# Kernel optimization log

Hardware: AMD Instinct MI355X
Metric: run time of the kernel (lower is better)

## Reference

```python
import math
import jax, jax.numpy as jnp
import numpy as np

DIM = 1024
N_HEADS = 16
N_KV_HEADS = 4
HEAD_DIM = 64
WINDOW = 512
EPS = 1e-6
B, S = 2, 2048

def _alibi_slopes(n_heads):
    def pow2(n):
        r = 2.0 ** (-8.0 / n)
        return np.array([r ** (i + 1) for i in range(n)], dtype=np.float32)
    if math.log2(n_heads).is_integer():
        return pow2(n_heads)
    m = 2 ** math.floor(math.log2(n_heads))
    return np.concatenate([pow2(m), pow2(2 * m)[::2][: n_heads - m]])

def _rmsnorm(x, w, eps=EPS):
    var = jnp.mean(x * x, axis=-1, keepdims=True)
    return x * jax.lax.rsqrt(var + eps) * w

def setup_inputs() -> dict:
    key = jax.random.key(0)
    ks = jax.random.split(key, 8)
    x = jax.random.normal(ks[0], (B, S, DIM), dtype=jnp.float32)
    wq = 0.02 * jax.random.normal(ks[1], (N_HEADS * HEAD_DIM, DIM), dtype=jnp.float32)
    wk = 0.02 * jax.random.normal(ks[2], (N_KV_HEADS * HEAD_DIM, DIM), dtype=jnp.float32)
    wv = 0.02 * jax.random.normal(ks[3], (N_KV_HEADS * HEAD_DIM, DIM), dtype=jnp.float32)
    wo = 0.02 * jax.random.normal(ks[4], (DIM, N_HEADS * HEAD_DIM), dtype=jnp.float32)
    q_norm_w = jnp.ones((N_HEADS * HEAD_DIM,), dtype=jnp.float32)
    k_norm_w = jnp.ones((N_KV_HEADS * HEAD_DIM,), dtype=jnp.float32)
    return {"x": x, "wq": wq, "wk": wk, "wv": wv, "wo": wo,
            "q_norm_w": q_norm_w, "k_norm_w": k_norm_w}

def reference(x, wq, wk, wv, wo, q_norm_w, k_norm_w):
    bsz, seqlen, _ = x.shape
    repeats = N_HEADS // N_KV_HEADS
    xq = _rmsnorm(x @ wq.T, q_norm_w)
    xk = _rmsnorm(x @ wk.T, k_norm_w)
    xv = x @ wv.T
    # [b, h, s, d]
    q = xq.reshape(bsz, seqlen, N_HEADS, HEAD_DIM).transpose(0, 2, 1, 3)
    k = xk.reshape(bsz, seqlen, N_KV_HEADS, HEAD_DIM).transpose(0, 2, 1, 3)
    v = xv.reshape(bsz, seqlen, N_KV_HEADS, HEAD_DIM).transpose(0, 2, 1, 3)
    k = jnp.repeat(k, repeats, axis=1)
    v = jnp.repeat(v, repeats, axis=1)
    pos = jnp.arange(seqlen)
    rel = pos[None, :] - pos[:, None]  # [s_q, s_k], key - query
    slopes = jnp.asarray(_alibi_slopes(N_HEADS))
    bias = slopes[:, None, None] * rel[None].astype(x.dtype)  # [h, s, s]
    masked = (rel > 0) | (rel < -WINDOW)  # causal + sliding window
    bias = jnp.where(masked[None], -jnp.inf, bias)
    scale = 1.0 / math.sqrt(HEAD_DIM)
    scores = jnp.einsum('bhqd,bhkd->bhqk', q, k) * scale + bias[None]
    probs = jax.nn.softmax(scores, axis=-1)
    y = jnp.einsum('bhqk,bhkd->bhqd', probs, v)
    y = y.transpose(0, 2, 1, 3).reshape(bsz, seqlen, N_HEADS * HEAD_DIM)
    return y @ wo.T
```

## Files before the change

### kernel.cpp

```cpp
#include <hip/hip_runtime.h>

typedef unsigned short u16;
typedef unsigned int u32;

typedef __bf16 bf16x8 __attribute__((ext_vector_type(8)));
typedef float f32x4 __attribute__((ext_vector_type(4)));

__device__ __forceinline__ u16 f2bf(float f) {
  u32 u = __builtin_bit_cast(u32, f);
  u32 r = (u + 0x7fffu + ((u >> 16) & 1u)) >> 16;
  return (u16)r;
}
__device__ __forceinline__ float bf2f(u16 v) {
  u32 u = (u32)v << 16;
  return __builtin_bit_cast(float, u);
}

__global__ __launch_bounds__(256)
void cvt_all_kernel(const float* __restrict__ x, const float* __restrict__ wq,
                    const float* __restrict__ wk, const float* __restrict__ wv,
                    const float* __restrict__ wo, u16* __restrict__ x_bf,
                    u16* __restrict__ wcat_bf, u16* __restrict__ wo_bf) {
  int t = blockIdx.x * 256 + threadIdx.x;
  const float* src;
  u16* dst;
  if (t < 1048576) {
    src = x; dst = x_bf;
  } else if (t < 1310720) {
    src = wq; dst = wcat_bf; t -= 1048576;
  } else if (t < 1376256) {
    src = wk; dst = wcat_bf + 1048576; t -= 1310720;
  } else if (t < 1441792) {
    src = wv; dst = wcat_bf + 1310720; t -= 1376256;
  } else {
    src = wo; dst = wo_bf; t -= 1441792;
  }
  const int i = t * 4;
  float4 v = *(const float4*)(src + i);
  uint2 p;
  p.x = (u32)f2bf(v.x) | ((u32)f2bf(v.y) << 16);
  p.y = (u32)f2bf(v.z) | ((u32)f2bf(v.w) << 16);
  *(uint2*)(dst + i) = p;
}

template <typename OutT>
__global__ __launch_bounds__(256)
void gemm_bt_kernel(const u16* __restrict__ A, const u16* __restrict__ B,
                    OutT* __restrict__ C, int M, int N, int K) {
  __shared__ u16 As[2][64 * 64];
  __shared__ u16 Bs[2][128 * 64];
  const int tid = threadIdx.x;
  const int lane = tid & 63;
  const int wave = tid >> 6;
  const int wm = (wave >> 1) * 32;
  const int wn = (wave & 1) * 64;
  const int l15 = lane & 15;
  const int quad = lane >> 4;
  const int sw = l15 & 7;
  const size_t bm = (size_t)blockIdx.y * 64;
  const size_t bn = (size_t)blockIdx.x * 128;

  f32x4 acc[2][4];
#pragma unroll
  for (int i = 0; i < 2; ++i)
#pragma unroll
    for (int j = 0; j < 4; ++j) acc[i][j] = f32x4{0.f, 0.f, 0.f, 0.f};

  const int ra0 = tid >> 3, ba0 = tid & 7;
  const int ra1 = (tid + 256) >> 3, ba1 = tid & 7;
  const u16* Ap0 = A + (bm + ra0) * (size_t)K + ba0 * 8;
  const u16* Ap1 = A + (bm + ra1) * (size_t)K + ba1 * 8;
  const u16* Bp0 = B + (bn + ra0) * (size_t)K + ba0 * 8;
  const u16* Bp1 = B + (bn + ra1) * (size_t)K + ba1 * 8;
  const u16* Bp2 = B + (bn + ra0 + 64) * (size_t)K + ba0 * 8;
  const u16* Bp3 = B + (bn + ra1 + 64) * (size_t)K + ba1 * 8;
  const int wa0 = ra0 * 64 + ((ba0 ^ (ra0 & 7)) * 8);
  const int wa1 = ra1 * 64 + ((ba1 ^ (ra1 & 7)) * 8);
  const int wb2 = (ra0 + 64) * 64 + ((ba0 ^ (ra0 & 7)) * 8);
  const int wb3 = (ra1 + 64) * 64 + ((ba1 ^ (ra1 & 7)) * 8);

  {
    uint4 a0 = *(const uint4*)Ap0, a1 = *(const uint4*)Ap1;
    uint4 b0 = *(const uint4*)Bp0, b1 = *(const uint4*)Bp1;
    uint4 b2 = *(const uint4*)Bp2, b3 = *(const uint4*)Bp3;
    *(uint4*)(&As[0][wa0]) = a0;
    *(uint4*)(&As[0][wa1]) = a1;
    *(uint4*)(&Bs[0][wa0]) = b0;
    *(uint4*)(&Bs[0][wa1]) = b1;
    *(uint4*)(&Bs[0][wb2]) = b2;
    *(uint4*)(&Bs[0][wb3]) = b3;
  }
  __syncthreads();

  int cur = 0;
  for (int k0 = 0; k0 < K; k0 += 64) {
    const int kn = (k0 + 64 < K) ? k0 + 64 : 0;
    uint4 a0 = *(const uint4*)(Ap0 + kn);
    uint4 a1 = *(const uint4*)(Ap1 + kn);
    uint4 b0 = *(const uint4*)(Bp0 + kn);
    uint4 b1 = *(const uint4*)(Bp1 + kn);
    uint4 b2 = *(const uint4*)(Bp2 + kn);
    uint4 b3 = *(const uint4*)(Bp3 + kn);

    const u16* Asc = As[cur];
    const u16* Bsc = Bs[cur];
#pragma unroll
    for (int h = 0; h < 2; ++h) {
      const int cb = quad + 4 * h;
      bf16x8 af[2], bfr[4];
#pragma unroll
      for (int i = 0; i < 2; ++i)
        af[i] = *(const bf16x8*)(&Asc[(wm + i * 16 + l15) * 64 + ((cb ^ sw) * 8)]);
#pragma unroll
      for (int j = 0; j < 4; ++j)
        bfr[j] = *(const bf16x8*)(&Bsc[(wn + j * 16 + l15) * 64 + ((cb ^ sw) * 8)]);
#pragma unroll
      for (int i = 0; i < 2; ++i)
#pragma unroll
        for (int j = 0; j < 4; ++j)
          acc[i][j] = __builtin_amdgcn_mfma_f32_16x16x32_bf16(af[i], bfr[j], acc[i][j], 0, 0, 0);
    }

    u16* Asn = As[cur ^ 1];
    u16* Bsn = Bs[cur ^ 1];
    *(uint4*)(&Asn[wa0]) = a0;
    *(uint4*)(&Asn[wa1]) = a1;
    *(uint4*)(&Bsn[wa0]) = b0;
    *(uint4*)(&Bsn[wa1]) = b1;
    *(uint4*)(&Bsn[wb2]) = b2;
    *(uint4*)(&Bsn[wb3]) = b3;
    __syncthreads();
    cur ^= 1;
  }

  const int rq = quad * 4;
#pragma unroll
  for (int i = 0; i < 2; ++i) {
#pragma unroll
    for (int r = 0; r < 4; ++r) {
      OutT* crow = C + (bm + wm + i * 16 + rq + r) * (size_t)N + bn + wn + l15;
#pragma unroll
      for (int j = 0; j < 4; ++j) {
        if constexpr (sizeof(OutT) == 2)
          crow[j * 16] = f2bf(acc[i][j][r]);
        else
          crow[j * 16] = acc[i][j][r];
      }
    }
  }
}

__global__ __launch_bounds__(256)
void norm_vtrans_kernel(u16* __restrict__ qkv, const float* __restrict__ qw,
                        const float* __restrict__ kw, u16* __restrict__ vt) {
  __shared__ u16 shmem[64 * 72];
  const int bid = blockIdx.x;
  const int tid = threadIdx.x;
  if (bid < 4096) {
    float* red = (float*)shmem;
    u16* row = qkv + (size_t)bid * 1536;
    uint2 pk = *(const uint2*)(row + tid * 4);
    float v0 = bf2f((u16)pk.x), v1 = bf2f((u16)(pk.x >> 16));
    float v2 = bf2f((u16)pk.y), v3 = bf2f((u16)(pk.y >> 16));
    float ss = v0 * v0 + v1 * v1 + v2 * v2 + v3 * v3;
#pragma unroll
    for (int off = 32; off > 0; off >>= 1) ss += __shfl_down(ss, off);
    if ((tid & 63) == 0) red[tid >> 6] = ss;
    __syncthreads();
    float tot = red[0] + red[1] + red[2] + red[3];
    float rn = rsqrtf(tot * (1.0f / 1024.0f) + 1e-6f);
    float4 w = *(const float4*)(qw + tid * 4);
    uint2 po;
    po.x = (u32)f2bf(v0 * rn * w.x) | ((u32)f2bf(v1 * rn * w.y) << 16);
    po.y = (u32)f2bf(v2 * rn * w.z) | ((u32)f2bf(v3 * rn * w.w) << 16);
    *(uint2*)(row + tid * 4) = po;
    if (tid < 64) {
      uint2 kp = *(const uint2*)(row + 1024 + tid * 4);
      float k0 = bf2f((u16)kp.x), k1 = bf2f((u16)(kp.x >> 16));
      float k2 = bf2f((u16)kp.y), k3 = bf2f((u16)(kp.y >> 16));
      float sk = k0 * k0 + k1 * k1 + k2 * k2 + k3 * k3;
#pragma unroll
      for (int off = 32; off > 0; off >>= 1) sk += __shfl_down(sk, off);
      float tk = __shfl(sk, 0);
      float rk = rsqrtf(tk * (1.0f / 256.0f) + 1e-6f);
      float4 w2 = *(const float4*)(kw + tid * 4);
      uint2 ko;
      ko.x = (u32)f2bf(k0 * rk * w2.x) | ((u32)f2bf(k1 * rk * w2.y) << 16);
      ko.y = (u32)f2bf(k2 * rk * w2.z) | ((u32)f2bf(k3 * rk * w2.w) << 16);
      *(uint2*)(row + 1024 + tid * 4) = ko;
    }
  } else {
    const int e = bid - 4096;
    const int t0 = (e & 31) * 64, kvh = (e >> 5) & 3, b = e >> 7;
    u16(*tile)[72] = (u16(*)[72])shmem;
    const int r = tid >> 2, c16 = (tid & 3) * 16;
    const u16* src = qkv + (size_t)(b * 2048 + t0 + r) * 1536 + 1280 + kvh * 64 + c16;
    *(uint4*)&tile[r][c16] = *(const uint4*)src;
    *(uint4*)&tile[r][c16 + 8] = *(const uint4*)(src + 8);
    __syncthreads();
    const int d = tid >> 2, t16 = (tid & 3) * 16;
    u16 o[16];
#pragma unroll
    for (int j = 0; j < 16; ++j) o[j] = tile[t16 + j][d];
    u16* dst = vt + (size_t)((b * 4 + kvh) * 64 + d) * 2048 + t0 + t16;
    *(uint4*)dst = *(uint4*)&o[0];
    *(uint4*)(dst + 8) = *(uint4*)&o[8];
  }
}

__global__ __launch_bounds__(512)
void attn_kernel(const u16* __restrict__ qkvbf, const u16* __restrict__ vt,
                 u16* __restrict__ ybf) {
  __shared__ u16 Ks[2][64 * 72];
  __shared__ u16 Vts[2][64 * 72];
  __shared__ u16 Ps[128 * 72];
  const int qt = blockIdx.x, h = blockIdx.y, b = blockIdx.z;
  const int kvh = h >> 2, q0 = qt * 128;
  const int tid = threadIdx.x, lane = tid & 63, w = tid >> 6;
  const int l15 = lane & 15, quad = lane >> 4;

  const u16* qrow = qkvbf + (size_t)(b * 2048 + q0 + w * 16 + l15) * 1536 + h * 64 + quad * 8;
  const bf16x8 qf0 = *(const bf16x8*)qrow;
  const bf16x8 qf1 = *(const bf16x8*)(qrow + 32);

  const int sr = tid >> 3, sc = (tid & 7) * 8;
  const u16* kbase = qkvbf + (size_t)(b * 2048 + sr) * 1536 + 1024 + kvh * 64 + sc;
  const u16* vbase = vt + (size_t)((b * 4 + kvh) * 64 + sr) * 2048 + sc;

  f32x4 O[4];
#pragma unroll
  for (int jd = 0; jd < 4; ++jd) O[jd] = f32x4{0.f, 0.f, 0.f, 0.f};
  float m_i = -1e30f, l_i = 0.f;
  const float LOG2E = 1.44269504f;
  const float sc2 = 0.125f * LOG2E;
  const float slope2 = exp2f(-0.5f * (float)(h + 1)) * LOG2E;
  const int c_lo = (q0 >= 512) ? (q0 - 512) : 0;
  const int c_hi = q0 + 64;
  const int myq_lo = q0 + w * 16;
  const int myq_hi = myq_lo + 15;
  const int myq = myq_lo + l15;

  {
    uint4 kr = *(const uint4*)(kbase + (size_t)c_lo * 1536);
    uint4 vr = *(const uint4*)(vbase + c_lo);
    *(uint4*)&Ks[0][sr * 72 + sc] = kr;
    *(uint4*)&Vts[0][sr * 72 + sc] = vr;
  }
  __syncthreads();

  int cur = 0;
  for (int c = c_lo; c <= c_hi; c += 64) {
    const int cn = (c + 64 <= c_hi) ? c + 64 : c_lo;
    uint4 kr = *(const uint4*)(kbase + (size_t)cn * 1536);
    uint4 vr = *(const uint4*)(vbase + cn);

    if (!(c > myq_hi || c + 63 < myq_lo - 512)) {
      const u16* Kc = Ks[cur];
      const u16* Vc = Vts[cur];
      f32x4 st[4];
#pragma unroll
      for (int i = 0; i < 4; ++i) {
        bf16x8 a0 = *(const bf16x8*)&Kc[(i * 16 + l15) * 72 + quad * 8];
        bf16x8 a1 = *(const bf16x8*)&Kc[(i * 16 + l15) * 72 + 32 + quad * 8];
        f32x4 z = f32x4{0.f, 0.f, 0.f, 0.f};
        z = __builtin_amdgcn_mfma_f32_16x16x32_bf16(a0, qf0, z, 0, 0, 0);
        st[i] = __builtin_amdgcn_mfma_f32_16x16x32_bf16(a1, qf1, z, 0, 0, 0);
      }

      float sv[4][4];
      float rm = -1e30f;
      const bool interior = (c + 63 <= myq_lo) && (c + 512 >= myq_hi);
      if (interior) {
#pragma unroll
        for (int i = 0; i < 4; ++i)
#pragma unroll
          for (int r = 0; r < 4; ++r) {
            const int key = c + i * 16 + quad * 4 + r;
            float val = st[i][r] * sc2 + slope2 * (float)(key - myq);
            sv[i][r] = val;
            rm = fmaxf(rm, val);
          }
      } else {
#pragma unroll
        for (int i = 0; i < 4; ++i)
#pragma unroll
          for (int r = 0; r < 4; ++r) {
            const int key = c + i * 16 + quad * 4 + r;
            const int rel = key - myq;
            float val = (rel > 0 || rel < -512) ? -1e30f
                                                : st[i][r] * sc2 + slope2 * (float)rel;
            sv[i][r] = val;
            rm = fmaxf(rm, val);
          }
      }
      rm = fmaxf(rm, __shfl_xor(rm, 16));
      rm = fmaxf(rm, __shfl_xor(rm, 32));
      const float mn = fmaxf(m_i, rm);
      const float alpha = exp2f(m_i - mn);
      float ls = 0.f;
#pragma unroll
      for (int i = 0; i < 4; ++i) {
        float p0 = exp2f(sv[i][0] - mn);
        float p1 = exp2f(sv[i][1] - mn);
        float p2 = exp2f(sv[i][2] - mn);
        float p3 = exp2f(sv[i][3] - mn);
        ls += (p0 + p1) + (p2 + p3);
        uint2 pw;
        pw.x = (u32)f2bf(p0) | ((u32)f2bf(p1) << 16);
        pw.y = (u32)f2bf(p2) | ((u32)f2bf(p3) << 16);
        *(uint2*)&Ps[(w * 16 + l15) * 72 + i * 16 + quad * 4] = pw;
      }
      ls += __shfl_xor(ls, 16);
      ls += __shfl_xor(ls, 32);
      l_i = l_i * alpha + ls;
      m_i = mn;

      float ar[4];
#pragma unroll
      for (int r = 0; r < 4; ++r) ar[r] = __shfl(alpha, quad * 4 + r);
#pragma unroll
      for (int jd = 0; jd < 4; ++jd)
#pragma unroll
        for (int r = 0; r < 4; ++r) O[jd][r] *= ar[r];

      bf16x8 pf0 = *(const bf16x8*)&Ps[(w * 16 + l15) * 72 + quad * 8];
      bf16x8 pf1 = *(const bf16x8*)&Ps[(w * 16 + l15) * 72 + 32 + quad * 8];
#pragma unroll
      for (int jd = 0; jd < 4; ++jd) {
        bf16x8 v0 = *(const bf16x8*)&Vc[(jd * 16 + l15) * 72 + quad * 8];
        bf16x8 v1 = *(const bf16x8*)&Vc[(jd * 16 + l15) * 72 + 32 + quad * 8];
        O[jd] = __builtin_amdgcn_mfma_f32_16x16x32_bf16(pf0, v0, O[jd], 0, 0, 0);
        O[jd] = __builtin_amdgcn_mfma_f32_16x16x32_bf16(pf1, v1, O[jd], 0, 0, 0);
      }
    }

    *(uint4*)&Ks[cur ^ 1][sr * 72 + sc] = kr;
    *(uint4*)&Vts[cur ^ 1][sr * 72 + sc] = vr;
    __syncthreads();
    cur ^= 1;
  }

  float lr[4];
#pragma unroll
  for (int r = 0; r < 4; ++r) lr[r] = __shfl(l_i, quad * 4 + r);
#pragma unroll
  for (int r = 0; r < 4; ++r) {
    const float inv = 1.0f / lr[r];
    u16* orow = ybf + (size_t)(b * 2048 + q0 + w * 16 + quad * 4 + r) * 1024 + h * 64 + l15;
#pragma unroll
    for (int jd = 0; jd < 4; ++jd) orow[jd * 16] = f2bf(O[jd][r] * inv);
  }
}

extern "C" void kernel_launch(void* const* d_in, const int* in_sizes, int n_in,
                              void* d_out, int out_size, void* d_ws, size_t ws_size,
                              hipStream_t stream) {
  const float* x = (const float*)d_in[0];
  const float* wq = (const float*)d_in[1];
  const float* wk = (const float*)d_in[2];
  const float* wv = (const float*)d_in[3];
  const float* wo = (const float*)d_in[4];
  const float* qnw = (const float*)d_in[5];
  const float* knw = (const float*)d_in[6];
  float* out = (float*)d_out;
  char* ws = (char*)d_ws;

  u16* x_bf = (u16*)(ws);
  u16* wcat_bf = (u16*)(ws + 8388608);
  u16* wo_bf = (u16*)(ws + 11534336);
  u16* qkv_bf = (u16*)(ws + 13631488);
  u16* vt_bf = (u16*)(ws + 26214400);
  u16* y_bf = (u16*)(ws + 28311552);

  cvt_all_kernel<<<6656, 256, 0, stream>>>(x, wq, wk, wv, wo, x_bf, wcat_bf, wo_bf);

  gemm_bt_kernel<u16><<<dim3(12, 64), 256, 0, stream>>>(x_bf, wcat_bf, qkv_bf, 4096, 1536, 1024);
  norm_vtrans_kernel<<<4352, 256, 0, stream>>>(qkv_bf, qnw, knw, vt_bf);
  attn_kernel<<<dim3(16, 16, 2), 512, 0, stream>>>(qkv_bf, vt_bf, y_bf);
  gemm_bt_kernel<float><<<dim3(8, 64), 256, 0, stream>>>(y_bf, wo_bf, out, 4096, 1024, 1024);
}
```

Before: 160.3 us.

## Switch attention to 32x32x16 MFMA with 4 waves of 32 query rows

The attention kernel now uses 32x32x16 bf16 MFMAs, with each wave owning 32 query rows and the block shrunk to 256 threads. This removes the cross-quad shuffles for the row max, row sum and alpha, and cuts LDS fragment reloads per MFMA. The output is staged through LDS so each lane writes 64-byte rows instead of scattered 2-byte stores. In exchange there are fewer waves per block and more accumulator registers per thread, which could lower occupancy or latency hiding.

```diff
diff --git a/kernel.cpp b/kernel.cpp
--- a/kernel.cpp
+++ b/kernel.cpp
@@ -5,6 +5,7 @@
 
 typedef __bf16 bf16x8 __attribute__((ext_vector_type(8)));
 typedef float f32x4 __attribute__((ext_vector_type(4)));
+typedef float f32x16 __attribute__((ext_vector_type(16)));
 
 __device__ __forceinline__ u16 f2bf(float f) {
   u32 u = __builtin_bit_cast(u32, f);
@@ -208,7 +209,7 @@
   }
 }
 
-__global__ __launch_bounds__(512)
+__global__ __launch_bounds__(256)
 void attn_kernel(const u16* __restrict__ qkvbf, const u16* __restrict__ vt,
                  u16* __restrict__ ybf) {
   __shared__ u16 Ks[2][64 * 72];
@@ -217,139 +218,160 @@
   const int qt = blockIdx.x, h = blockIdx.y, b = blockIdx.z;
   const int kvh = h >> 2, q0 = qt * 128;
   const int tid = threadIdx.x, lane = tid & 63, w = tid >> 6;
-  const int l15 = lane & 15, quad = lane >> 4;
-
-  const u16* qrow = qkvbf + (size_t)(b * 2048 + q0 + w * 16 + l15) * 1536 + h * 64 + quad * 8;
-  const bf16x8 qf0 = *(const bf16x8*)qrow;
-  const bf16x8 qf1 = *(const bf16x8*)(qrow + 32);
-
-  const int sr = tid >> 3, sc = (tid & 7) * 8;
+  const int l31 = lane & 31, half = lane >> 5;
+  const int h8 = half * 8, h4 = half * 4;
+
+  const int myq = q0 + w * 32 + l31;
+  const u16* qrow = qkvbf + (size_t)(b * 2048 + myq) * 1536 + h * 64 + h8;
+  bf16x8 qf[4];
+#pragma unroll
+  for (int s = 0; s < 4; ++s) qf[s] = *(const bf16x8*)(qrow + s * 16);
+
+  const int sr = tid >> 2, sc = (tid & 3) * 16;
   const u16* kbase = qkvbf + (size_t)(b * 2048 + sr) * 1536 + 1024 + kvh * 64 + sc;
   const u16* vbase = vt + (size_t)((b * 4 + kvh) * 64 + sr) * 2048 + sc;
 
-  f32x4 O[4];
-#pragma unroll
-  for (int jd = 0; jd < 4; ++jd) O[jd] = f32x4{0.f, 0.f, 0.f, 0.f};
+  f32x16 Ot[2];
+#pragma unroll
+  for (int t = 0; t < 2; ++t)
+#pragma unroll
+    for (int e = 0; e < 16; ++e) Ot[t][e] = 0.f;
   float m_i = -1e30f, l_i = 0.f;
   const float LOG2E = 1.44269504f;
   const float sc2 = 0.125f * LOG2E;
   const float slope2 = exp2f(-0.5f * (float)(h + 1)) * LOG2E;
   const int c_lo = (q0 >= 512) ? (q0 - 512) : 0;
   const int c_hi = q0 + 64;
-  const int myq_lo = q0 + w * 16;
-  const int myq_hi = myq_lo + 15;
-  const int myq = myq_lo + l15;
+  const int myq_lo = q0 + w * 32;
+  const int myq_hi = myq_lo + 31;
 
   {
-    uint4 kr = *(const uint4*)(kbase + (size_t)c_lo * 1536);
-    uint4 vr = *(const uint4*)(vbase + c_lo);
-    *(uint4*)&Ks[0][sr * 72 + sc] = kr;
-    *(uint4*)&Vts[0][sr * 72 + sc] = vr;
+    uint4 k0 = *(const uint4*)(kbase + (size_t)c_lo * 1536);
+    uint4 k1 = *(const uint4*)(kbase + (size_t)c_lo * 1536 + 8);
+    uint4 v0 = *(const uint4*)(vbase + c_lo);
+    uint4 v1 = *(const uint4*)(vbase + c_lo + 8);
+    *(uint4*)&Ks[0][sr * 72 + sc] = k0;
+    *(uint4*)&Ks[0][sr * 72 + sc + 8] = k1;
+    *(uint4*)&Vts[0][sr * 72 + sc] = v0;
+    *(uint4*)&Vts[0][sr * 72 + sc + 8] = v1;
   }
   __syncthreads();
 
   int cur = 0;
   for (int c = c_lo; c <= c_hi; c += 64) {
     const int cn = (c + 64 <= c_hi) ? c + 64 : c_lo;
-    uint4 kr = *(const uint4*)(kbase + (size_t)cn * 1536);
-    uint4 vr = *(const uint4*)(vbase + cn);
+    uint4 kr0 = *(const uint4*)(kbase + (size_t)cn * 1536);
+    uint4 kr1 = *(const uint4*)(kbase + (size_t)cn * 1536 + 8);
+    uint4 vr0 = *(const uint4*)(vbase + cn);
+    uint4 vr1 = *(const uint4*)(vbase + cn + 8);
 
     if (!(c > myq_hi || c + 63 < myq_lo - 512)) {
       const u16* Kc = Ks[cur];
       const u16* Vc = Vts[cur];
-      f32x4 st[4];
-#pragma unroll
-      for (int i = 0; i < 4; ++i) {
-        bf16x8 a0 = *(const bf16x8*)&Kc[(i * 16 + l15) * 72 + quad * 8];
-        bf16x8 a1 = *(const bf16x8*)&Kc[(i * 16 + l15) * 72 + 32 + quad * 8];
-        f32x4 z = f32x4{0.f, 0.f, 0.f, 0.f};
-        z = __builtin_amdgcn_mfma_f32_16x16x32_bf16(a0, qf0, z, 0, 0, 0);
-        st[i] = __builtin_amdgcn_mfma_f32_16x16x32_bf16(a1, qf1, z, 0, 0, 0);
+      f32x16 st[2];
+#pragma unroll
+      for (int i = 0; i < 2; ++i) {
+#pragma unroll
+        for (int e = 0; e < 16; ++e) st[i][e] = 0.f;
+#pragma unroll
+        for (int s = 0; s < 4; ++s) {
+          bf16x8 a = *(const bf16x8*)&Kc[(i * 32 + l31) * 72 + s * 16 + h8];
+          st[i] = __builtin_amdgcn_mfma_f32_32x32x16_bf16(a, qf[s], st[i], 0, 0, 0);
+        }
       }
-
-      float sv[4][4];
       float rm = -1e30f;
       const bool interior = (c + 63 <= myq_lo) && (c + 512 >= myq_hi);
       if (interior) {
 #pragma unroll
-        for (int i = 0; i < 4; ++i)
-#pragma unroll
-          for (int r = 0; r < 4; ++r) {
-            const int key = c + i * 16 + quad * 4 + r;
+        for (int i = 0; i < 2; ++i)
+#pragma unroll
+          for (int r = 0; r < 16; ++r) {
+            const int key = c + i * 32 + (r & 3) + 8 * (r >> 2) + h4;
             float val = st[i][r] * sc2 + slope2 * (float)(key - myq);
-            sv[i][r] = val;
+            st[i][r] = val;
             rm = fmaxf(rm, val);
           }
       } else {
 #pragma unroll
-        for (int i = 0; i < 4; ++i)
-#pragma unroll
-          for (int r = 0; r < 4; ++r) {
-            const int key = c + i * 16 + quad * 4 + r;
+        for (int i = 0; i < 2; ++i)
+#pragma unroll
+          for (int r = 0; r < 16; ++r) {
+            const int key = c + i * 32 + (r & 3) + 8 * (r >> 2) + h4;
             const int rel = key - myq;
             float val = (rel > 0 || rel < -512) ? -1e30f
                                                 : st[i][r] * sc2 + slope2 * (float)rel;
-            sv[i][r] = val;
+            st[i][r] = val;
             rm = fmaxf(rm, val);
           }
       }
-      rm = fmaxf(rm, __shfl_xor(rm, 16));
       rm = fmaxf(rm, __shfl_xor(rm, 32));
       const float mn = fmaxf(m_i, rm);
       const float alpha = exp2f(m_i - mn);
       float ls = 0.f;
 #pragma unroll
-      for (int i = 0; i < 4; ++i) {
-        float p0 = exp2f(sv[i][0] - mn);
-        float p1 = exp2f(sv[i][1] - mn);
-        float p2 = exp2f(sv[i][2] - mn);
-        float p3 = exp2f(sv[i][3] - mn);
-        ls += (p0 + p1) + (p2 + p3);
-        uint2 pw;
-        pw.x = (u32)f2bf(p0) | ((u32)f2bf(p1) << 16);
-        pw.y = (u32)f2bf(p2) | ((u32)f2bf(p3) << 16);
-        *(uint2*)&Ps[(w * 16 + l15) * 72 + i * 16 + quad * 4] = pw;
+      for (int i = 0; i < 2; ++i) {
+#pragma unroll
+        for (int rg = 0; rg < 4; ++rg) {
+          float p0 = exp2f(st[i][rg * 4 + 0] - mn);
+          float p1 = exp2f(st[i][rg * 4 + 1] - mn);
+          float p2 = exp2f(st[i][rg * 4 + 2] - mn);
+          float p3 = exp2f(st[i][rg * 4 + 3] - mn);
+          ls += (p0 + p1) + (p2 + p3);
+          uint2 pw;
+          pw.x = (u32)f2bf(p0) | ((u32)f2bf(p1) << 16);
+          pw.y = (u32)f2bf(p2) | ((u32)f2bf(p3) << 16);
+          *(uint2*)&Ps[(w * 32 + l31) * 72 + i * 32 + rg * 8 + h4] = pw;
+        }
       }
-      ls += __shfl_xor(ls, 16);
       ls += __shfl_xor(ls, 32);
       l_i = l_i * alpha + ls;
       m_i = mn;
-
-      float ar[4];
-#pragma unroll
-      for (int r = 0; r < 4; ++r) ar[r] = __shfl(alpha, quad * 4 + r);
-#pragma unroll
-      for (int jd = 0; jd < 4; ++jd)
-#pragma unroll
-        for (int r = 0; r < 4; ++r) O[jd][r] *= ar[r];
-
-      bf16x8 pf0 = *(const bf16x8*)&Ps[(w * 16 + l15) * 72 + quad * 8];
-      bf16x8 pf1 = *(const bf16x8*)&Ps[(w * 16 + l15) * 72 + 32 + quad * 8];
-#pragma unroll
-      for (int jd = 0; jd < 4; ++jd) {
-        bf16x8 v0 = *(const bf16x8*)&Vc[(jd * 16 + l15) * 72 + quad * 8];
-        bf16x8 v1 = *(const bf16x8*)&Vc[(jd * 16 + l15) * 72 + 32 + quad * 8];
-        O[jd] = __builtin_amdgcn_mfma_f32_16x16x32_bf16(pf0, v0, O[jd], 0, 0, 0);
-        O[jd] = __builtin_amdgcn_mfma_f32_16x16x32_bf16(pf1, v1, O[jd], 0, 0, 0);
-      }
+#pragma unroll
+      for (int t = 0; t < 2; ++t)
+#pragma unroll
+        for (int e = 0; e < 16; ++e) Ot[t][e] *= alpha;
+      bf16x8 pf[4];
+#pragma unroll
+      for (int s = 0; s < 4; ++s)
+        pf[s] = *(const bf16x8*)&Ps[(w * 32 + l31) * 72 + s * 16 + h8];
+#pragma unroll
+      for (int t = 0; t < 2; ++t)
+#pragma unroll
+        for (int s = 0; s < 4; ++s) {
+          bf16x8 a = *(const bf16x8*)&Vc[(t * 32 + l31) * 72 + s * 16 + h8];
+          Ot[t] = __builtin_amdgcn_mfma_f32_32x32x16_bf16(a, pf[s], Ot[t], 0, 0, 0);
+        }
     }
 
-    *(uint4*)&Ks[cur ^ 1][sr * 72 + sc] = kr;
-    *(uint4*)&Vts[cur ^ 1][sr * 72 + sc] = vr;
+    *(uint4*)&Ks[cur ^ 1][sr * 72 + sc] = kr0;
+    *(uint4*)&Ks[cur ^ 1][sr * 72 + sc + 8] = kr1;
+    *(uint4*)&Vts[cur ^ 1][sr * 72 + sc] = vr0;
+    *(uint4*)&Vts[cur ^ 1][sr * 72 + sc + 8] = vr1;
     __syncthreads();
     cur ^= 1;
   }
 
-  float lr[4];
-#pragma unroll
-  for (int r = 0; r < 4; ++r) lr[r] = __shfl(l_i, quad * 4 + r);
-#pragma unroll
-  for (int r = 0; r < 4; ++r) {
-    const float inv = 1.0f / lr[r];
-    u16* orow = ybf + (size_t)(b * 2048 + q0 + w * 16 + quad * 4 + r) * 1024 + h * 64 + l15;
-#pragma unroll
-    for (int jd = 0; jd < 4; ++jd) orow[jd * 16] = f2bf(O[jd][r] * inv);
-  }
+  const float inv = 1.0f / l_i;
+#pragma unroll
+  for (int t = 0; t < 2; ++t)
+#pragma unroll
+    for (int rg = 0; rg < 4; ++rg) {
+      uint2 ow;
+      ow.x = (u32)f2bf(Ot[t][rg * 4 + 0] * inv) | ((u32)f2bf(Ot[t][rg * 4 + 1] * inv) << 16);
+      ow.y = (u32)f2bf(Ot[t][rg * 4 + 2] * inv) | ((u32)f2bf(Ot[t][rg * 4 + 3] * inv) << 16);
+      *(uint2*)&Ps[(w * 32 + l31) * 72 + t * 32 + rg * 8 + h4] = ow;
+    }
+  const int qr = lane >> 1, dh = (lane & 1) * 32;
+  const u16* prow = &Ps[(w * 32 + qr) * 72 + dh];
+  uint4 o0 = *(const uint4*)(prow);
+  uint4 o1 = *(const uint4*)(prow + 8);
+  uint4 o2 = *(const uint4*)(prow + 16);
+  uint4 o3 = *(const uint4*)(prow + 24);
+  u16* orow = ybf + (size_t)(b * 2048 + q0 + w * 32 + qr) * 1024 + h * 64 + dh;
+  *(uint4*)(orow) = o0;
+  *(uint4*)(orow + 8) = o1;
+  *(uint4*)(orow + 16) = o2;
+  *(uint4*)(orow + 24) = o3;
 }
 
 extern "C" void kernel_launch(void* const* d_in, const int* in_sizes, int n_in,
@@ -376,6 +398,6 @@
 
   gemm_bt_kernel<u16><<<dim3(12, 64), 256, 0, stream>>>(x_bf, wcat_bf, qkv_bf, 4096, 1536, 1024);
   norm_vtrans_kernel<<<4352, 256, 0, stream>>>(qkv_bf, qnw, knw, vt_bf);
-  attn_kernel<<<dim3(16, 16, 2), 512, 0, stream>>>(qkv_bf, vt_bf, y_bf);
+  attn_kernel<<<dim3(16, 16, 2), 256, 0, stream>>>(qkv_bf, vt_bf, y_bf);
   gemm_bt_kernel<float><<<dim3(8, 64), 256, 0, stream>>>(y_bf, wo_bf, out, 4096, 1024, 1024);
 }
```

After: 163.2 us. No clear change (+1.8%).
